# Kernel tuning notes

Hardware: AMD Instinct MI355X
Metric: run time of the kernel (lower is better)

Reference implementation:

```python
import jax, jax.numpy as jnp
import numpy as np

B, D, O = 65536, 512, 64   # batch, input_size, output_size
E, T, K = 8, 2, 2          # num_experts, n_task, top-k
H1, H2 = 64, 32            # expert_hidden_layers (hardcoded in Expert)
LOSS_COEF = 0.01
EPS = 1e-10


def setup_inputs() -> dict:
    key = jax.random.key(0)
    ks = jax.random.split(key, 8)
    f32 = jnp.float32
    def rn(k, shape, scale):
        return jax.random.normal(k, shape, f32) * scale
    return {
        "x": jax.random.normal(ks[0], (B, D), f32),
        # gating params (one per task); init random so top-k routing is nontrivial
        "w_gates": rn(ks[1], (T, D, E), 0.02),
        "b_gates": jnp.zeros((T, E), f32),
        # per-expert MLP params, stacked over the expert axis
        "W1": rn(ks[2], (E, D, H1), 1.0 / np.sqrt(D)),
        "b1": jnp.zeros((E, H1), f32),
        "W2": rn(ks[3], (E, H1, H2), 1.0 / np.sqrt(H1)),
        "b2": jnp.zeros((E, H2), f32),
        "W3": rn(ks[4], (E, H2, O), 1.0 / np.sqrt(H2)),
        "b3": jnp.zeros((E, O), f32),
    }


def _cv_squared(v):
    # torch .var() default is unbiased (ddof=1)
    return jnp.var(v, ddof=1) / (jnp.mean(v) ** 2 + EPS)


def reference(x, w_gates, b_gates, W1, b1, W2, b2, W3, b3):
    # --- noisy_top_k_gating in eval mode (train=False): clean logits, top-k softmax ---
    logits = jnp.einsum("bd,tde->tbe", x, w_gates) + b_gates[:, None, :]  # [T,B,E]
    top_v, top_i = jax.lax.top_k(logits, K)                                # [T,B,K]
    top_g = jax.nn.softmax(top_v, axis=-1)                                 # [T,B,K]
    # scatter top-k gate values back to dense [T,B,E] (zeros elsewhere)
    gates = jnp.sum(jax.nn.one_hot(top_i, E, dtype=top_g.dtype) * top_g[..., None], axis=2)

    # --- experts: each token through each expert MLP (gates zero out non-selected,
    #     mathematically identical to dispatch/combine) ---
    h = jax.nn.relu(jnp.einsum("bd,edh->ebh", x, W1) + b1[:, None, :])     # [E,B,H1]
    h = jax.nn.relu(jnp.einsum("ebh,eho->ebo", h, W2) + b2[:, None, :])    # [E,B,H2]
    expert_out = jax.nn.relu(jnp.einsum("ebh,eho->ebo", h, W3) + b3[:, None, :])  # [E,B,O]

    # weighted combine per task
    y = jnp.einsum("tbe,ebo->tbo", gates, expert_out)                       # [T,B,O]

    # --- load balancing loss ---
    importance = gates.sum(axis=1)                          # [T,E]
    load = (gates > 0).sum(axis=1).astype(jnp.float32)      # [T,E]
    loss = LOSS_COEF * (jax.vmap(_cv_squared)(importance) + jax.vmap(_cv_squared)(load)).sum()
    return y, loss
```

## Files before the change

### kernel.cpp

```cpp
#include <hip/hip_runtime.h>


typedef short bfrag __attribute__((ext_vector_type(8)));
typedef float facc  __attribute__((ext_vector_type(4)));

#define MFMA16(a, b, c) __builtin_amdgcn_mfma_f32_16x16x32_bf16((a), (b), (c), 0, 0, 0)

__device__ __forceinline__ unsigned short bfbits(float f) {
  unsigned int u = __builtin_bit_cast(unsigned int, f);
  u += 0x7FFFu + ((u >> 16) & 1u);
  return (unsigned short)(u >> 16);
}
__device__ __forceinline__ unsigned pack2(float a, float b) {
  return (unsigned)bfbits(a) | ((unsigned)bfbits(b) << 16);
}
__device__ __forceinline__ float bf2f(unsigned short s) {
  unsigned int u = ((unsigned int)s) << 16;
  return __builtin_bit_cast(float, u);
}

#define GG_OFF   65536
#define GL_OFF   70656
#define GSM_SIZE 70784

__global__ __launch_bounds__(1024, 4) void moe_gate(
    const float* __restrict__ x,
    const float* __restrict__ b_gates,
    const float* __restrict__ wgt,
    float4* __restrict__ routing,
    float* __restrict__ gacc,
    float* __restrict__ y)
{
  __shared__ alignas(16) char gsm[GSM_SIZE];
  const int tid = threadIdx.x;
  const int wave = tid >> 6, lane = tid & 63;

  const float* src = x + (size_t)blockIdx.x * 64 * 512 + lane * 512 + wave * 32;
  float4 fr[8];
  #pragma unroll
  for (int j = 0; j < 8; ++j) fr[j] = ((const float4*)src)[j];

  if (tid < 32) ((float*)(gsm + GL_OFF))[tid] = 0.f;

  {
    int wu = __builtin_amdgcn_readfirstlane(wave);
    const float* wbase = wgt + wu * 32;
    float* pp = (float*)(gsm + wave * 4096 + lane * 64);
    #pragma unroll
    for (int te = 0; te < 16; ++te) {
      const float* wrow = wbase + te * 512;
      float a0 = 0.f, a1 = 0.f, a2 = 0.f, a3 = 0.f;
      #pragma unroll
      for (int j = 0; j < 8; ++j) {
        a0 = fmaf(fr[j].x, wrow[j * 4 + 0], a0);
        a1 = fmaf(fr[j].y, wrow[j * 4 + 1], a1);
        a2 = fmaf(fr[j].z, wrow[j * 4 + 2], a2);
        a3 = fmaf(fr[j].w, wrow[j * 4 + 3], a3);
      }
      pp[(te + lane) & 15] = (a0 + a1) + (a2 + a3);
    }
  }
  __syncthreads();

  {
    int tok = tid >> 4, te = tid & 15;
    const char* pb = gsm + tok * 64 + (((te + tok) & 15) * 4);
    float s = 0.f;
    #pragma unroll
    for (int w2 = 0; w2 < 16; ++w2) s += *(const float*)(pb + w2 * 4096);
    ((float*)(gsm + GG_OFF))[tok * 20 + te] = s + b_gates[te];
  }
  __syncthreads();

  if (tid < 128) {
    int tok = tid >> 1, task = tid & 1;
    const float* Gr = (const float*)(gsm + GG_OFF) + tok * 20 + task * 8;
    float l[8];
    #pragma unroll
    for (int ee = 0; ee < 8; ++ee) l[ee] = Gr[ee];
    float v1 = l[0]; int e1 = 0;
    #pragma unroll
    for (int ee = 1; ee < 8; ++ee) { if (l[ee] > v1) { v1 = l[ee]; e1 = ee; } }
    float v2 = -3.4e38f; int e2 = 0;
    #pragma unroll
    for (int ee = 0; ee < 8; ++ee) {
      if (ee != e1 && l[ee] > v2) { v2 = l[ee]; e2 = ee; }
    }
    float g1 = 1.f / (1.f + __expf(v2 - v1));
    float g2 = 1.f - g1;
    float4 rec;
    rec.x = g1; rec.y = g2;
    rec.z = __int_as_float(e1); rec.w = __int_as_float(e2);
    routing[((size_t)blockIdx.x * 64 + tok) * 2 + task] = rec;
    float* lacc = (float*)(gsm + GL_OFF);
    atomicAdd(lacc + task * 8 + e1, g1);
    atomicAdd(lacc + task * 8 + e2, g2);
    atomicAdd(lacc + 16 + task * 8 + e1, 1.f);
    atomicAdd(lacc + 16 + task * 8 + e2, 1.f);
  }
  __syncthreads();
  if (tid < 32) atomicAdd(gacc + tid, ((float*)(gsm + GL_OFF))[tid]);
  __syncthreads();

  if (tid == 0) {
    unsigned* cnt = (unsigned*)(gacc + 32);
    unsigned old = atomicAdd(cnt, 1u);
    if (old == gridDim.x - 1) {
      float loss = 0.f;
      #pragma unroll
      for (int a = 0; a < 4; ++a) {
        float v[8]; float mm = 0.f;
        #pragma unroll
        for (int i = 0; i < 8; ++i) {
          v[i] = __hip_atomic_load(gacc + a * 8 + i, __ATOMIC_RELAXED,
                                   __HIP_MEMORY_SCOPE_AGENT);
          mm += v[i];
        }
        mm *= 0.125f;
        float var = 0.f;
        #pragma unroll
        for (int i = 0; i < 8; ++i) { float d = v[i] - mm; var += d * d; }
        loss += (var * (1.f / 7.f)) / (mm * mm + 1e-10f);
      }
      y[8388608] = 0.01f * loss;
    }
  }
}

__global__ __launch_bounds__(512, 6) void moe_main(
    const float* __restrict__ x,
    const float* __restrict__ b1,
    const float* __restrict__ b2,
    const float* __restrict__ b3,
    const bfrag* __restrict__ w1f,
    const bfrag* __restrict__ w2f,
    const bfrag* __restrict__ w3f,
    const float4* __restrict__ routing,
    float* __restrict__ y)
{
  __shared__ alignas(16) char smem[32768];
  const int tid = threadIdx.x;
  const int wave = tid >> 6, lane = tid & 63;
  const int q = lane & 15, g = lane >> 4;
  const int e = wave;
  const unsigned cb = (unsigned)e * 4096u;

  {
    const float* xblk = x + (size_t)blockIdx.x * 32 * 512;
    #pragma unroll 4
    for (int it = 0; it < 8; ++it) {
      int idx = it * 2048 + tid * 4;
      float4 v = *(const float4*)(xblk + idx);
      int r = idx >> 9, c = idx & 511;
      unsigned byte = ((unsigned)(r * 1024 + c * 2)) ^ ((unsigned)(r & 7) << 4);
      uint2 p; p.x = pack2(v.x, v.y); p.y = pack2(v.z, v.w);
      *(uint2*)(smem + byte) = p;
    }
  }
  __syncthreads();

  facc acc[2][4];
  #pragma unroll
  for (int m = 0; m < 2; ++m)
    #pragma unroll
    for (int n = 0; n < 4; ++n) acc[m][n] = (facc)0.f;

  const bfrag* w1e = w1f + e * 4096 + lane;
  #pragma unroll
  for (int ks = 0; ks < 16; ++ks) {
    bfrag B0 = w1e[ks * 256];
    bfrag B1 = w1e[ks * 256 + 64];
    bfrag B2 = w1e[ks * 256 + 128];
    bfrag B3 = w1e[ks * 256 + 192];
    #pragma unroll
    for (int m = 0; m < 2; ++m) {
      unsigned ba = ((unsigned)((m * 16 + q) * 1024 + ks * 64 + g * 16)) ^ ((unsigned)(q & 7) << 4);
      bfrag A = *(const bfrag*)(smem + ba);
      acc[m][0] = MFMA16(A, B0, acc[m][0]);
      acc[m][1] = MFMA16(A, B1, acc[m][1]);
      acc[m][2] = MFMA16(A, B2, acc[m][2]);
      acc[m][3] = MFMA16(A, B3, acc[m][3]);
    }
  }

  bfrag W2r[4];
  #pragma unroll
  for (int i = 0; i < 4; ++i) W2r[i] = w2f[e * 256 + i * 64 + lane];
  float b2v0 = b2[e * 32 + q];
  float b2v1 = b2[e * 32 + 16 + q];
  __syncthreads();

  {
    float bv[4];
    #pragma unroll
    for (int n = 0; n < 4; ++n) bv[n] = b1[e * 64 + n * 16 + q];
    #pragma unroll
    for (int m = 0; m < 2; ++m) {
      #pragma unroll
      for (int j = 0; j < 4; ++j) {
        float v0 = fmaxf(acc[m][0][j] + bv[0], 0.f);
        float v1 = fmaxf(acc[m][1][j] + bv[1], 0.f);
        float v2 = fmaxf(acc[m][2][j] + bv[2], 0.f);
        float v3 = fmaxf(acc[m][3][j] + bv[3], 0.f);
        int rr = m * 16 + g * 4 + j;
        unsigned byte = cb + (((unsigned)(rr * 128 + q * 8)) ^ ((unsigned)(rr & 7) << 4));
        uint2 pk; pk.x = pack2(v0, v1); pk.y = pack2(v2, v3);
        *(uint2*)(smem + byte) = pk;
      }
    }
  }

  {
    facc a2[2][2];
    #pragma unroll
    for (int m = 0; m < 2; ++m) { a2[m][0] = (facc)0.f; a2[m][1] = (facc)0.f; }
    #pragma unroll
    for (int ks = 0; ks < 2; ++ks) {
      #pragma unroll
      for (int m = 0; m < 2; ++m) {
        unsigned ba = cb + (((unsigned)((m * 16 + q) * 128 + ks * 64 + g * 16)) ^ ((unsigned)(q & 7) << 4));
        bfrag A = *(const bfrag*)(smem + ba);
        a2[m][0] = MFMA16(A, W2r[ks * 2], a2[m][0]);
        a2[m][1] = MFMA16(A, W2r[ks * 2 + 1], a2[m][1]);
      }
    }
    bfrag W3r[4];
    #pragma unroll
    for (int n = 0; n < 4; ++n) W3r[n] = w3f[e * 256 + n * 64 + lane];
    float b3v[4];
    #pragma unroll
    for (int n = 0; n < 4; ++n) b3v[n] = b3[e * 64 + n * 16 + q];

    #pragma unroll
    for (int m = 0; m < 2; ++m) {
      #pragma unroll
      for (int j = 0; j < 4; ++j) {
        float v0 = fmaxf(a2[m][0][j] + b2v0, 0.f);
        float v1 = fmaxf(a2[m][1][j] + b2v1, 0.f);
        int rr = m * 16 + g * 4 + j;
        unsigned byte = cb + (((unsigned)(rr * 64 + q * 4)) ^ ((unsigned)(rr & 7) << 4));
        *(unsigned int*)(smem + byte) = pack2(v0, v1);
      }
    }

    facc a3[2][4];
    #pragma unroll
    for (int m = 0; m < 2; ++m)
      #pragma unroll
      for (int n = 0; n < 4; ++n) a3[m][n] = (facc)0.f;
    #pragma unroll
    for (int m = 0; m < 2; ++m) {
      unsigned ba = cb + (((unsigned)((m * 16 + q) * 64 + g * 16)) ^ ((unsigned)(q & 7) << 4));
      bfrag A = *(const bfrag*)(smem + ba);
      #pragma unroll
      for (int n = 0; n < 4; ++n) a3[m][n] = MFMA16(A, W3r[n], a3[m][n]);
    }
    #pragma unroll
    for (int m = 0; m < 2; ++m) {
      #pragma unroll
      for (int j = 0; j < 4; ++j) {
        float v0 = fmaxf(a3[m][0][j] + b3v[0], 0.f);
        float v1 = fmaxf(a3[m][1][j] + b3v[1], 0.f);
        float v2 = fmaxf(a3[m][2][j] + b3v[2], 0.f);
        float v3 = fmaxf(a3[m][3][j] + b3v[3], 0.f);
        int rr = m * 16 + g * 4 + j;
        unsigned byte = cb + (((unsigned)(rr * 128 + q * 8)) ^ ((unsigned)(rr & 7) << 4));
        uint2 pk; pk.x = pack2(v0, v1); pk.y = pack2(v2, v3);
        *(uint2*)(smem + byte) = pk;
      }
    }
  }
  __syncthreads();

  {
    int tok = tid >> 4, u = tid & 15;
    size_t trow = (size_t)blockIdx.x * 32 + tok;
    unsigned obyte = ((unsigned)(tok * 128 + u * 8)) ^ ((unsigned)(tok & 7) << 4);
    #pragma unroll
    for (int tt = 0; tt < 2; ++tt) {
      float4 rec = routing[trow * 2 + tt];
      float g1 = rec.x, g2 = rec.y;
      int e1 = __float_as_int(rec.z), e2 = __float_as_int(rec.w);
      uint2 o1 = *(const uint2*)(smem + e1 * 4096 + obyte);
      uint2 o2 = *(const uint2*)(smem + e2 * 4096 + obyte);
      unsigned short s1[4] = { (unsigned short)o1.x, (unsigned short)(o1.x >> 16),
                               (unsigned short)o1.y, (unsigned short)(o1.y >> 16) };
      unsigned short s2[4] = { (unsigned short)o2.x, (unsigned short)(o2.x >> 16),
                               (unsigned short)o2.y, (unsigned short)(o2.y >> 16) };
      float* yt = y + (size_t)tt * 4194304 + trow * 64;
      #pragma unroll
      for (int w = 0; w < 4; ++w) {
        yt[w * 16 + u] = g1 * bf2f(s1[w]) + g2 * bf2f(s2[w]);
      }
    }
  }
}

__global__ __launch_bounds__(256) void moe_prep(
    const float* __restrict__ W1, const float* __restrict__ W2,
    const float* __restrict__ W3, const float* __restrict__ wg,
    bfrag* __restrict__ w1f, bfrag* __restrict__ w2f,
    bfrag* __restrict__ w3f, float* __restrict__ wgt,
    float* __restrict__ gacc)
{
  int tid = blockIdx.x * 256 + threadIdx.x;
  bfrag o;
  if (tid < 32768) {
    int lane = tid & 63, nt = (tid >> 6) & 3, ks = (tid >> 8) & 15, e = tid >> 12;
    int q = lane & 15, g = lane >> 4;
    int hcol = nt * 16 + q;
    #pragma unroll
    for (int j = 0; j < 8; ++j) {
      int k = ks * 32 + g * 8 + j;
      o[j] = (short)bfbits(W1[((e * 512 + k) * 64) + hcol]);
    }
    w1f[tid] = o;
  } else if (tid < 34816) {
    int idx = tid - 32768;
    int lane = idx & 63, nt = (idx >> 6) & 1, ks = (idx >> 7) & 1, e = idx >> 8;
    int q = lane & 15, g = lane >> 4;
    int n = nt * 16 + q;
    #pragma unroll
    for (int j = 0; j < 8; ++j) {
      int s = ks * 32 + g * 8 + j;
      int hh = (s & 3) * 16 + (s >> 2);
      o[j] = (short)bfbits(W2[(e * 64 + hh) * 32 + n]);
    }
    w2f[idx] = o;
  } else if (tid < 36864) {
    int idx = tid - 34816;
    int lane = idx & 63, nt = (idx >> 6) & 3, e = idx >> 8;
    int q = lane & 15, g = lane >> 4;
    int ocol = nt * 16 + q;
    #pragma unroll
    for (int j = 0; j < 8; ++j) {
      int s = g * 8 + j;
      int hh = (s & 1) * 16 + (s >> 1);
      o[j] = (short)bfbits(W3[(e * 32 + hh) * 64 + ocol]);
    }
    w3f[idx] = o;
  } else if (tid < 45056) {
    int idx = tid - 36864;
    int te = idx >> 9, k = idx & 511;
    wgt[idx] = wg[(((te >> 3) * 512) + k) * 8 + (te & 7)];
  } else if (tid < 45089) {
    gacc[tid - 45056] = 0.f;
  }
}

extern "C" void kernel_launch(void* const* d_in, const int* in_sizes, int n_in,
                              void* d_out, int out_size, void* d_ws, size_t ws_size,
                              hipStream_t stream) {
  const float* x  = (const float*)d_in[0];
  const float* wg = (const float*)d_in[1];
  const float* bg = (const float*)d_in[2];
  const float* W1 = (const float*)d_in[3];
  const float* b1 = (const float*)d_in[4];
  const float* W2 = (const float*)d_in[5];
  const float* b2 = (const float*)d_in[6];
  const float* W3 = (const float*)d_in[7];
  const float* b3 = (const float*)d_in[8];
  float* y = (float*)d_out;

  char* ws = (char*)d_ws;
  float*  gacc    = (float*)ws;
  bfrag*  w1f     = (bfrag*)(ws + 256);
  bfrag*  w2f     = (bfrag*)(ws + 524544);
  bfrag*  w3f     = (bfrag*)(ws + 557312);
  float*  wgt     = (float*)(ws + 590080);
  float4* routing = (float4*)(ws + 622848);

  moe_prep<<<177, 256, 0, stream>>>(W1, W2, W3, wg, w1f, w2f, w3f, wgt, gacc);
  moe_gate<<<1024, 1024, 0, stream>>>(x, bg, wgt, routing, gacc, y);
  moe_main<<<2048, 512, 0, stream>>>(x, b1, b2, b3, w1f, w2f, w3f, routing, y);
}
```

Measured before the change: 104.1 us.

## Emit pre-swizzled bf16 copy of x from gate kernel for main kernel

```diff
diff --git a/kernel.cpp b/kernel.cpp
--- a/kernel.cpp
+++ b/kernel.cpp
@@ -5,6 +5,9 @@
 typedef float facc  __attribute__((ext_vector_type(4)));
 
 #define MFMA16(a, b, c) __builtin_amdgcn_mfma_f32_16x16x32_bf16((a), (b), (c), 0, 0, 0)
+
+typedef const __attribute__((address_space(1))) unsigned int guint;
+typedef __attribute__((address_space(3))) unsigned int luint;
 
 __device__ __forceinline__ unsigned short bfbits(float f) {
   unsigned int u = __builtin_bit_cast(unsigned int, f);
@@ -23,13 +26,15 @@
 #define GL_OFF   70656
 #define GSM_SIZE 70784
 
+template <int XBF>
 __global__ __launch_bounds__(1024, 4) void moe_gate(
     const float* __restrict__ x,
     const float* __restrict__ b_gates,
     const float* __restrict__ wgt,
     float4* __restrict__ routing,
     float* __restrict__ gacc,
-    float* __restrict__ y)
+    float* __restrict__ y,
+    char* __restrict__ xbf)
 {
   __shared__ alignas(16) char gsm[GSM_SIZE];
   const int tid = threadIdx.x;
@@ -71,6 +76,21 @@
     ((float*)(gsm + GG_OFF))[tok * 20 + te] = s + b_gates[te];
   }
   __syncthreads();
+
+  if (XBF) {
+    int sub = lane >> 5, r = lane & 31;
+    #pragma unroll
+    for (int p = 0; p < 4; ++p) {
+      uint4 v;
+      v.x = pack2(fr[2 * p].x, fr[2 * p].y);
+      v.y = pack2(fr[2 * p].z, fr[2 * p].w);
+      v.z = pack2(fr[2 * p + 1].x, fr[2 * p + 1].y);
+      v.w = pack2(fr[2 * p + 1].z, fr[2 * p + 1].w);
+      unsigned byte = (unsigned)(sub * 32768) +
+                      (((unsigned)(r * 1024 + wave * 64 + p * 16)) ^ ((unsigned)(r & 7) << 4));
+      *(uint4*)(gsm + byte) = v;
+    }
+  }
 
   if (tid < 128) {
     int tok = tid >> 1, task = tid & 1;
@@ -99,10 +119,20 @@
     atomicAdd(lacc + 16 + task * 8 + e2, 1.f);
   }
   __syncthreads();
+
+  if (XBF) {
+    char* dst = xbf + (size_t)blockIdx.x * 65536;
+    #pragma unroll
+    for (int it = 0; it < 4; ++it) {
+      int off = it * 16384 + tid * 16;
+      *(uint4*)(dst + off) = *(const uint4*)(gsm + off);
+    }
+  }
   if (tid < 32) atomicAdd(gacc + tid, ((float*)(gsm + GL_OFF))[tid]);
   __syncthreads();
 
   if (tid == 0) {
+    __threadfence();
     unsigned* cnt = (unsigned*)(gacc + 32);
     unsigned old = atomicAdd(cnt, 1u);
     if (old == gridDim.x - 1) {
@@ -127,8 +157,10 @@
   }
 }
 
+template <int XBF>
 __global__ __launch_bounds__(512, 6) void moe_main(
     const float* __restrict__ x,
+    const char* __restrict__ xbf,
     const float* __restrict__ b1,
     const float* __restrict__ b2,
     const float* __restrict__ b3,
@@ -145,7 +177,14 @@
   const int e = wave;
   const unsigned cb = (unsigned)e * 4096u;
 
-  {
+  if (XBF) {
+    const char* src = xbf + (size_t)blockIdx.x * 32768;
+    #pragma unroll
+    for (int it = 0; it < 4; ++it) {
+      int off = it * 8192 + tid * 16;
+      __builtin_amdgcn_global_load_lds((guint*)(src + off), (luint*)(smem + off), 16, 0, 0);
+    }
+  } else {
     const float* xblk = x + (size_t)blockIdx.x * 32 * 512;
     #pragma unroll 4
     for (int it = 0; it < 8; ++it) {
@@ -369,8 +408,15 @@
   bfrag*  w3f     = (bfrag*)(ws + 557312);
   float*  wgt     = (float*)(ws + 590080);
   float4* routing = (float4*)(ws + 622848);
+  char*   xbf     = ws + 2752512;
+  const bool use_xbf = ws_size >= (size_t)2752512 + 67108864;
 
   moe_prep<<<177, 256, 0, stream>>>(W1, W2, W3, wg, w1f, w2f, w3f, wgt, gacc);
-  moe_gate<<<1024, 1024, 0, stream>>>(x, bg, wgt, routing, gacc, y);
-  moe_main<<<2048, 512, 0, stream>>>(x, b1, b2, b3, w1f, w2f, w3f, routing, y);
-}
+  if (use_xbf) {
+    moe_gate<1><<<1024, 1024, 0, stream>>>(x, bg, wgt, routing, gacc, y, xbf);
+    moe_main<1><<<2048, 512, 0, stream>>>(x, xbf, b1, b2, b3, w1f, w2f, w3f, routing, y);
+  } else {
+    moe_gate<0><<<1024, 1024, 0, stream>>>(x, bg, wgt, routing, gacc, y, xbf);
+    moe_main<0><<<2048, 512, 0, stream>>>(x, xbf, b1, b2, b3, w1f, w2f, w3f, routing, y);
+  }
+}
```

After: 138.2 us. 1.33x slower.
